# Performance work log

Measured on AMD Instinct MI355X. Metric: run time of the kernel, lower is better.

Reference implementation:

```python
import jax, jax.numpy as jnp
import numpy as np

K = 3
STRIDE = 1


def ste_round(v):
    # Round with straight-through gradient (torch Round Function)
    return v + jax.lax.stop_gradient(jnp.round(v) - v)


def ste_sign(v):
    # Sign with straight-through gradient (torch Sign Function)
    return v + jax.lax.stop_gradient(jnp.sign(v) - v)


def _unfold(x, k, s):
    # torch nn.functional.unfold: [B,C,H,W] -> [B, C*k*k, L], channel-major (c, kh, kw)
    B, C, H, W = x.shape
    Ho = (H - k) // s + 1
    Wo = (W - k) // s + 1
    cols = jnp.stack(
        [x[:, :, i:i + s * Ho:s, j:j + s * Wo:s] for i in range(k) for j in range(k)],
        axis=2,
    )  # [B, C, k*k, Ho, Wo]
    return cols.reshape(B, C * k * k, Ho * Wo)


def reference(x, weight, conv_bias, in_min, in_max, prob_table, rand_idx):
    B = x.shape[0]
    O = weight.shape[0]
    cols = _unfold(x, K, STRIDE)                       # [B, CKK, L]
    CKK = cols.shape[1]
    X = cols.transpose(0, 2, 1).reshape(-1, CKK)       # [N, CKK], N = B*L

    w = ste_sign(weight.reshape(O, CKK))               # ternary weights {-1,0,1}
    wp = jax.nn.relu(w)
    wm = jax.nn.relu(-w)

    scale = in_max - in_min
    Xq = jnp.clip(ste_round((X - in_min) / scale * 15.0), 0.0, 15.0)

    nch = -(-CKK // 4)                                 # ceil(CKK/4)
    pad = nch * 4 - CKK
    if pad:
        Xq = jnp.pad(Xq, ((0, 0), (0, pad)))
        wp = jnp.pad(wp, ((0, 0), (0, pad)))
        wm = jnp.pad(wm, ((0, 0), (0, pad)))

    Xc = Xq.reshape(-1, nch, 4)                        # [N, nch, 4]
    Wp = wp.reshape(O, nch, 4)
    Wm = wm.reshape(O, nch, 4)

    yp = jnp.einsum('nck,ock->cno', Xc, Wp)            # [nch, N, O]
    ym = -jnp.einsum('nck,ock->cno', Xc, Wm)
    T = jnp.stack([yp, ym], axis=1)                    # [nch, 2, N, O]

    longs = jnp.abs(jnp.clip(jnp.round(T), -60.0, 60.0).astype(jnp.int32))
    Q = jnp.clip(ste_round(T / 15.0), -3.0, 3.0)
    temp = prob_table[longs, rand_idx]                 # irregular gather [nch,2,N,O]
    add = temp * jnp.sign(Q) + Q - jax.lax.stop_gradient(Q)

    bias_term = in_min * jnp.sum(w, axis=1)            # linear(InMin*ones, w) -> [O]
    xo = jnp.sum(add, axis=(0, 1)) * scale + bias_term + conv_bias  # [N, O]

    L = X.shape[0] // B
    dim = int(np.sqrt(L))
    return xo.reshape(B, L, O).transpose(0, 2, 1).reshape(B, O, dim, dim)


def setup_inputs() -> dict:
    key = jax.random.key(0)
    k1, k2, k3, k4, k5 = jax.random.split(key, 5)
    B, C, H, W = 2, 16, 66, 66
    O = 64
    CKK = C * K * K            # 144
    nch = -(-CKK // 4)         # 36
    L = ((H - K) // STRIDE + 1) ** 2  # 4096
    N = B * L                  # 8192
    return {
        'x': jax.random.uniform(k1, (B, C, H, W), dtype=jnp.float32),
        'weight': jax.random.normal(k2, (O, C, K, K), dtype=jnp.float32),
        'conv_bias': jax.random.normal(k3, (O,), dtype=jnp.float32),
        'in_min': jnp.zeros((), dtype=jnp.float32),
        'in_max': jnp.ones((), dtype=jnp.float32),
        'prob_table': jax.random.uniform(k4, (61, 1000), dtype=jnp.float32),
        'rand_idx': jax.random.randint(k5, (nch, 2, N, O), 0, 1000, dtype=jnp.int32),
    }
```

## Files before the change

kernel.cpp:

```cpp
#include <hip/hip_runtime.h>

typedef unsigned int uint;

#define B_     2
#define C_     16
#define H_     66
#define W_     66
#define O_     64
#define CKK    144
#define NCH    36
#define DIM    64
#define L_     4096
#define N_     8192
#define PLANE  524288
#define TROWS  61
#define TCOLS  1000

typedef _Float16 h4 __attribute__((ext_vector_type(4)));

__device__ __forceinline__ void loadg(int (&buf)[16],
                                      const int* __restrict__ rp0,
                                      const int* __restrict__ rp1, int c0) {
#pragma unroll
    for (int j = 0; j < 4; ++j) {
        int c = c0 + j;
        buf[4 * j + 0] = rp0[(2 * c)     * PLANE];
        buf[4 * j + 1] = rp0[(2 * c + 1) * PLANE];
        buf[4 * j + 2] = rp1[(2 * c)     * PLANE];
        buf[4 * j + 3] = rp1[(2 * c + 1) * PLANE];
    }
}

__device__ __forceinline__ void procg(const int (&buf)[16],
                                      const uint* __restrict__ xq0,
                                      const uint* __restrict__ xq1,
                                      const uint2* __restrict__ sw,
                                      const _Float16* __restrict__ tbl,
                                      int c0, int o,
                                      float& sum0, float& sum1) {
#pragma unroll
    for (int j = 0; j < 4; ++j) {
        int c = c0 + j;
        uint xv0 = xq0[c];
        uint xv1 = xq1[c];
        uint2 m  = sw[c * O_ + o];
        uint yp0 = ((xv0 & m.x) * 0x01010101u) >> 24;
        uint ym0 = ((xv0 & m.y) * 0x01010101u) >> 24;
        uint yp1 = ((xv1 & m.x) * 0x01010101u) >> 24;
        uint ym1 = ((xv1 & m.y) * 0x01010101u) >> 24;
        sum0 += (float)tbl[yp0 * TCOLS + buf[4 * j + 0]];
        sum0 -= (float)tbl[ym0 * TCOLS + buf[4 * j + 1]];
        sum1 += (float)tbl[yp1 * TCOLS + buf[4 * j + 2]];
        sum1 -= (float)tbl[ym1 * TCOLS + buf[4 * j + 3]];
    }
}

__launch_bounds__(1024)
__global__ void k_fused(const float* __restrict__ x,
                        const float* __restrict__ wgt,
                        const float* __restrict__ cbias,
                        const float* __restrict__ pmin,
                        const float* __restrict__ pmax,
                        const float* __restrict__ ptbl,
                        const int*   __restrict__ ridx,
                        float* __restrict__ out) {
    __shared__ __align__(16) _Float16 tbl[TROWS * TCOLS];
    __shared__ uint2 s_w[NCH * O_];
    __shared__ float s_bias[O_];
    __shared__ uint  s_xq[2][16 * NCH];

    const int tid = threadIdx.x;
    const float mn = pmin[0];
    const float sc = pmax[0] - mn;

    {
        uint4 z; z.x = z.y = z.z = z.w = 0u;
        uint4* zp = (uint4*)tbl;
        for (int p = tid; p < 1000; p += 1024) zp[p] = z;
    }
    {
        const float4* src = (const float4*)(ptbl + 8 * TCOLS);
        h4* dst = (h4*)(tbl + 8 * TCOLS);
        for (int p = tid; p < (53 * TCOLS) / 4; p += 1024) {
            float4 v = src[p];
            h4 h = { (_Float16)v.x, (_Float16)v.y, (_Float16)v.z, (_Float16)v.w };
            dst[p] = h;
        }
    }
    for (int p = tid; p < NCH * O_; p += 1024) {
        int c = p >> 6, oo = p & 63;
        float4 v = *(const float4*)(wgt + oo * CKK + c * 4);
        uint pm = 0, nm = 0;
        if (v.x > 0.0f) pm |= 0x000000FFu; else if (v.x < 0.0f) nm |= 0x000000FFu;
        if (v.y > 0.0f) pm |= 0x0000FF00u; else if (v.y < 0.0f) nm |= 0x0000FF00u;
        if (v.z > 0.0f) pm |= 0x00FF0000u; else if (v.z < 0.0f) nm |= 0x00FF0000u;
        if (v.w > 0.0f) pm |= 0xFF000000u; else if (v.w < 0.0f) nm |= 0xFF000000u;
        s_w[p] = make_uint2(pm, nm);
    }
    for (int i = tid; i < 2 * 16 * NCH; i += 1024) {
        int t  = i / (16 * NCH);
        int r  = i - t * (16 * NCH);
        int nl2 = r / NCH;
        int c2  = r - nl2 * NCH;
        int n2  = (blockIdx.x + t * 256) * 16 + nl2;
        int b2 = n2 >> 12, l2 = n2 & (L_ - 1);
        int h2 = l2 >> 6,  w2 = l2 & (DIM - 1);
        uint packed = 0;
#pragma unroll
        for (int k = 0; k < 4; ++k) {
            int j  = c2 * 4 + k;
            int ci = j / 9;
            int r2 = j - ci * 9;
            int kh = r2 / 3;
            int kw = r2 - kh * 3;
            float v = x[((b2 * C_ + ci) * H_ + (h2 + kh)) * W_ + (w2 + kw)];
            float t2 = (v - mn) / sc * 15.0f;
            float q = fminf(fmaxf(rintf(t2), 0.0f), 15.0f);
            packed |= ((uint)q) << (8 * k);
        }
        s_xq[t][r] = packed;
    }

    const int o  = tid & 63;
    const int nl = tid >> 6;
    const int n0 = blockIdx.x * 16 + nl;
    const int n1 = n0 + 4096;
    const int* rp0 = ridx + n0 * O_ + o;
    const int* rp1 = ridx + n1 * O_ + o;

    int A[16], Bb[16];
    loadg(A,  rp0, rp1, 0);
    loadg(Bb, rp0, rp1, 4);

    __syncthreads();
    if (tid < O_) {
        int sw2 = 0;
        for (int c = 0; c < NCH; ++c) {
            uint2 m = s_w[c * O_ + tid];
            sw2 += (__popc(m.x) >> 3) - (__popc(m.y) >> 3);
        }
        s_bias[tid] = mn * (float)sw2 + cbias[tid];
    }
    __syncthreads();

    const uint* xq0 = &s_xq[0][nl * NCH];
    const uint* xq1 = &s_xq[1][nl * NCH];
    const float bo  = s_bias[o];
    float sum0 = 0.0f, sum1 = 0.0f;

    procg(A,  xq0, xq1, s_w, tbl,  0, o, sum0, sum1); loadg(A,  rp0, rp1,  8);
    procg(Bb, xq0, xq1, s_w, tbl,  4, o, sum0, sum1); loadg(Bb, rp0, rp1, 12);
    procg(A,  xq0, xq1, s_w, tbl,  8, o, sum0, sum1); loadg(A,  rp0, rp1, 16);
    procg(Bb, xq0, xq1, s_w, tbl, 12, o, sum0, sum1); loadg(Bb, rp0, rp1, 20);
    procg(A,  xq0, xq1, s_w, tbl, 16, o, sum0, sum1); loadg(A,  rp0, rp1, 24);
    procg(Bb, xq0, xq1, s_w, tbl, 20, o, sum0, sum1); loadg(Bb, rp0, rp1, 28);
    procg(A,  xq0, xq1, s_w, tbl, 24, o, sum0, sum1); loadg(A,  rp0, rp1, 32);
    procg(Bb, xq0, xq1, s_w, tbl, 28, o, sum0, sum1);
    procg(A,  xq0, xq1, s_w, tbl, 32, o, sum0, sum1);

    out[o * L_ + n0]                       = sum0 * sc + bo;
    out[(O_ + o) * L_ + (n1 & (L_ - 1))]   = sum1 * sc + bo;
}

extern "C" void kernel_launch(void* const* d_in, const int* in_sizes, int n_in,
                              void* d_out, int out_size, void* d_ws, size_t ws_size,
                              hipStream_t stream) {
    const float* x     = (const float*)d_in[0];
    const float* wgt   = (const float*)d_in[1];
    const float* cbias = (const float*)d_in[2];
    const float* pmin  = (const float*)d_in[3];
    const float* pmax  = (const float*)d_in[4];
    const float* ptbl  = (const float*)d_in[5];
    const int*   ridx  = (const int*)d_in[6];
    float* out = (float*)d_out;

    k_fused<<<256, 1024, 0, stream>>>(x, wgt, cbias, pmin, pmax, ptbl, ridx, out);
}
```

Measured before the change: 34.90 us.

## Remap threads to two output channels each and vectorize rand_idx loads

Each thread now handles two adjacent output channels for one position instead of one channel for two batch positions. This lets the rand_idx gathers become int2 loads and the weight masks be packed as uint4 in shared memory. The prefetch depth grows from two to four register buffers, and the rand_idx loads are issued before the table setup to overlap the global latency with shared-memory initialization. The output stores become strided across channels per thread and register pressure increases.

```diff
diff --git a/kernel.cpp b/kernel.cpp
--- a/kernel.cpp
+++ b/kernel.cpp
@@ -18,40 +18,36 @@
 
 typedef _Float16 h4 __attribute__((ext_vector_type(4)));
 
-__device__ __forceinline__ void loadg(int (&buf)[16],
-                                      const int* __restrict__ rp0,
-                                      const int* __restrict__ rp1, int c0) {
+__device__ __forceinline__ void loadg(int2 (&buf)[8],
+                                      const int* __restrict__ rp, int c0) {
 #pragma unroll
     for (int j = 0; j < 4; ++j) {
         int c = c0 + j;
-        buf[4 * j + 0] = rp0[(2 * c)     * PLANE];
-        buf[4 * j + 1] = rp0[(2 * c + 1) * PLANE];
-        buf[4 * j + 2] = rp1[(2 * c)     * PLANE];
-        buf[4 * j + 3] = rp1[(2 * c + 1) * PLANE];
+        buf[2 * j + 0] = *(const int2*)(rp + (2 * c)     * PLANE);
+        buf[2 * j + 1] = *(const int2*)(rp + (2 * c + 1) * PLANE);
     }
 }
 
-__device__ __forceinline__ void procg(const int (&buf)[16],
-                                      const uint* __restrict__ xq0,
-                                      const uint* __restrict__ xq1,
-                                      const uint2* __restrict__ sw,
+__device__ __forceinline__ void procg(const int2 (&buf)[8],
+                                      const uint*  __restrict__ xqp,
+                                      const uint4* __restrict__ swp,
                                       const _Float16* __restrict__ tbl,
-                                      int c0, int o,
-                                      float& sum0, float& sum1) {
+                                      int c0, float& sum0, float& sum1) {
 #pragma unroll
     for (int j = 0; j < 4; ++j) {
         int c = c0 + j;
-        uint xv0 = xq0[c];
-        uint xv1 = xq1[c];
-        uint2 m  = sw[c * O_ + o];
-        uint yp0 = ((xv0 & m.x) * 0x01010101u) >> 24;
-        uint ym0 = ((xv0 & m.y) * 0x01010101u) >> 24;
-        uint yp1 = ((xv1 & m.x) * 0x01010101u) >> 24;
-        uint ym1 = ((xv1 & m.y) * 0x01010101u) >> 24;
-        sum0 += (float)tbl[yp0 * TCOLS + buf[4 * j + 0]];
-        sum0 -= (float)tbl[ym0 * TCOLS + buf[4 * j + 1]];
-        sum1 += (float)tbl[yp1 * TCOLS + buf[4 * j + 2]];
-        sum1 -= (float)tbl[ym1 * TCOLS + buf[4 * j + 3]];
+        uint  xv = xqp[c];
+        uint4 m  = swp[c * 32];
+        uint yp0 = ((xv & m.x) * 0x01010101u) >> 24;
+        uint ym0 = ((xv & m.y) * 0x01010101u) >> 24;
+        uint yp1 = ((xv & m.z) * 0x01010101u) >> 24;
+        uint ym1 = ((xv & m.w) * 0x01010101u) >> 24;
+        int2 b0 = buf[2 * j + 0];
+        int2 b1 = buf[2 * j + 1];
+        sum0 += (float)tbl[yp0 * TCOLS + b0.x];
+        sum0 -= (float)tbl[ym0 * TCOLS + b1.x];
+        sum1 += (float)tbl[yp1 * TCOLS + b0.y];
+        sum1 -= (float)tbl[ym1 * TCOLS + b1.y];
     }
 }
 
@@ -65,44 +61,69 @@
                         const int*   __restrict__ ridx,
                         float* __restrict__ out) {
     __shared__ __align__(16) _Float16 tbl[TROWS * TCOLS];
-    __shared__ uint2 s_w[NCH * O_];
+    __shared__ uint4 s_w4[NCH * 32];
     __shared__ float s_bias[O_];
     __shared__ uint  s_xq[2][16 * NCH];
 
-    const int tid = threadIdx.x;
+    const int tid  = threadIdx.x;
+    const int wv   = tid >> 6;
+    const int lane = tid & 63;
+    const int p    = lane & 31;
+    const int h    = lane >> 5;
+    const int s    = wv >> 3;
+    const int nloc = 2 * (wv & 7) + h;
+    const int o0   = 2 * p;
+
     const float mn = pmin[0];
     const float sc = pmax[0] - mn;
+
+    const int n_g = blockIdx.x * 16 + nloc + s * 4096;
+    const int* rp = ridx + n_g * O_ + o0;
+    int2 A[8], Bb[8], Cc[8], Dd[8];
+    loadg(A,  rp, 0);
+    loadg(Bb, rp, 4);
+    loadg(Cc, rp, 8);
+    loadg(Dd, rp, 12);
 
     {
         uint4 z; z.x = z.y = z.z = z.w = 0u;
         uint4* zp = (uint4*)tbl;
-        for (int p = tid; p < 1000; p += 1024) zp[p] = z;
+        for (int q = tid; q < 1000; q += 1024) zp[q] = z;
     }
     {
         const float4* src = (const float4*)(ptbl + 8 * TCOLS);
         h4* dst = (h4*)(tbl + 8 * TCOLS);
-        for (int p = tid; p < (53 * TCOLS) / 4; p += 1024) {
-            float4 v = src[p];
-            h4 h = { (_Float16)v.x, (_Float16)v.y, (_Float16)v.z, (_Float16)v.w };
-            dst[p] = h;
+        for (int q = tid; q < (53 * TCOLS) / 4; q += 1024) {
+            float4 v = src[q];
+            h4 hh = { (_Float16)v.x, (_Float16)v.y, (_Float16)v.z, (_Float16)v.w };
+            dst[q] = hh;
         }
     }
-    for (int p = tid; p < NCH * O_; p += 1024) {
-        int c = p >> 6, oo = p & 63;
-        float4 v = *(const float4*)(wgt + oo * CKK + c * 4);
+    for (int q = tid; q < NCH * 32; q += 1024) {
+        int c = q >> 5, pp = q & 31;
+        uint4 mo;
+        float4 v0 = *(const float4*)(wgt + (2 * pp)     * CKK + c * 4);
+        float4 v1 = *(const float4*)(wgt + (2 * pp + 1) * CKK + c * 4);
         uint pm = 0, nm = 0;
-        if (v.x > 0.0f) pm |= 0x000000FFu; else if (v.x < 0.0f) nm |= 0x000000FFu;
-        if (v.y > 0.0f) pm |= 0x0000FF00u; else if (v.y < 0.0f) nm |= 0x0000FF00u;
-        if (v.z > 0.0f) pm |= 0x00FF0000u; else if (v.z < 0.0f) nm |= 0x00FF0000u;
-        if (v.w > 0.0f) pm |= 0xFF000000u; else if (v.w < 0.0f) nm |= 0xFF000000u;
-        s_w[p] = make_uint2(pm, nm);
+        if (v0.x > 0.0f) pm |= 0x000000FFu; else if (v0.x < 0.0f) nm |= 0x000000FFu;
+        if (v0.y > 0.0f) pm |= 0x0000FF00u; else if (v0.y < 0.0f) nm |= 0x0000FF00u;
+        if (v0.z > 0.0f) pm |= 0x00FF0000u; else if (v0.z < 0.0f) nm |= 0x00FF0000u;
+        if (v0.w > 0.0f) pm |= 0xFF000000u; else if (v0.w < 0.0f) nm |= 0xFF000000u;
+        mo.x = pm; mo.y = nm;
+        pm = 0; nm = 0;
+        if (v1.x > 0.0f) pm |= 0x000000FFu; else if (v1.x < 0.0f) nm |= 0x000000FFu;
+        if (v1.y > 0.0f) pm |= 0x0000FF00u; else if (v1.y < 0.0f) nm |= 0x0000FF00u;
+        if (v1.z > 0.0f) pm |= 0x00FF0000u; else if (v1.z < 0.0f) nm |= 0x00FF0000u;
+        if (v1.w > 0.0f) pm |= 0xFF000000u; else if (v1.w < 0.0f) nm |= 0xFF000000u;
+        mo.z = pm; mo.w = nm;
+        s_w4[c * 32 + pp] = mo;
     }
     for (int i = tid; i < 2 * 16 * NCH; i += 1024) {
         int t  = i / (16 * NCH);
         int r  = i - t * (16 * NCH);
         int nl2 = r / NCH;
         int c2  = r - nl2 * NCH;
-        int n2  = (blockIdx.x + t * 256) * 16 + nl2;
+        int n2  = blockIdx.x * 16 + nl2 + t * 4096;
         int b2 = n2 >> 12, l2 = n2 & (L_ - 1);
         int h2 = l2 >> 6,  w2 = l2 & (DIM - 1);
         uint packed = 0;
@@ -120,46 +141,37 @@
         }
         s_xq[t][r] = packed;
     }
+    __syncthreads();
 
-    const int o  = tid & 63;
-    const int nl = tid >> 6;
-    const int n0 = blockIdx.x * 16 + nl;
-    const int n1 = n0 + 4096;
-    const int* rp0 = ridx + n0 * O_ + o;
-    const int* rp1 = ridx + n1 * O_ + o;
-
-    int A[16], Bb[16];
-    loadg(A,  rp0, rp1, 0);
-    loadg(Bb, rp0, rp1, 4);
-
-    __syncthreads();
-    if (tid < O_) {
-        int sw2 = 0;
+    if (tid < 32) {
+        int sw0 = 0, sw1 = 0;
         for (int c = 0; c < NCH; ++c) {
-            uint2 m = s_w[c * O_ + tid];
-            sw2 += (__popc(m.x) >> 3) - (__popc(m.y) >> 3);
+            uint4 m = s_w4[c * 32 + tid];
+            sw0 += (__popc(m.x) >> 3) - (__popc(m.y) >> 3);
+            sw1 += (__popc(m.z) >> 3) - (__popc(m.w) >> 3);
         }
-        s_bias[tid] = mn * (float)sw2 + cbias[tid];
+        s_bias[2 * tid]     = mn * (float)sw0 + cbias[2 * tid];
+        s_bias[2 * tid + 1] = mn * (float)sw1 + cbias[2 * tid + 1];
     }
     __syncthreads();
 
-    const uint* xq0 = &s_xq[0][nl * NCH];
-    const uint* xq1 = &s_xq[1][nl * NCH];
-    const float bo  = s_bias[o];
+    const uint*  xqp = &s_xq[s][nloc * NCH];
+    const uint4* swp = &s_w4[p];
     float sum0 = 0.0f, sum1 = 0.0f;
 
-    procg(A,  xq0, xq1, s_w, tbl,  0, o, sum0, sum1); loadg(A,  rp0, rp1,  8);
-    procg(Bb, xq0, xq1, s_w, tbl,  4, o, sum0, sum1); loadg(Bb, rp0, rp1, 12);
-    procg(A,  xq0, xq1, s_w, tbl,  8, o, sum0, sum1); loadg(A,  rp0, rp1, 16);
-    procg(Bb, xq0, xq1, s_w, tbl, 12, o, sum0, sum1); loadg(Bb, rp0, rp1, 20);
-    procg(A,  xq0, xq1, s_w, tbl, 16, o, sum0, sum1); loadg(A,  rp0, rp1, 24);
-    procg(Bb, xq0, xq1, s_w, tbl, 20, o, sum0, sum1); loadg(Bb, rp0, rp1, 28);
-    procg(A,  xq0, xq1, s_w, tbl, 24, o, sum0, sum1); loadg(A,  rp0, rp1, 32);
-    procg(Bb, xq0, xq1, s_w, tbl, 28, o, sum0, sum1);
-    procg(A,  xq0, xq1, s_w, tbl, 32, o, sum0, sum1);
+    procg(A,  xqp, swp, tbl,  0, sum0, sum1); loadg(A,  rp, 16);
+    procg(Bb, xqp, swp, tbl,  4, sum0, sum1); loadg(Bb, rp, 20);
+    procg(Cc, xqp, swp, tbl,  8, sum0, sum1); loadg(Cc, rp, 24);
+    procg(Dd, xqp, swp, tbl, 12, sum0, sum1); loadg(Dd, rp, 28);
+    procg(A,  xqp, swp, tbl, 16, sum0, sum1); loadg(A,  rp, 32);
+    procg(Bb, xqp, swp, tbl, 20, sum0, sum1);
+    procg(Cc, xqp, swp, tbl, 24, sum0, sum1);
+    procg(Dd, xqp, swp, tbl, 28, sum0, sum1);
+    procg(A,  xqp, swp, tbl, 32, sum0, sum1);
 
-    out[o * L_ + n0]                       = sum0 * sc + bo;
-    out[(O_ + o) * L_ + (n1 & (L_ - 1))]   = sum1 * sc + bo;
+    const int l = blockIdx.x * 16 + nloc;
+    out[(s * O_ + o0)     * L_ + l] = sum0 * sc + s_bias[o0];
+    out[(s * O_ + o0 + 1) * L_ + l] = sum1 * sc + s_bias[o0 + 1];
 }
 
 extern "C" void kernel_launch(void* const* d_in, const int* in_sizes, int n_in,
```

Result: slower. 36.54 us (+4.7%).

## Deepen rand_idx prefetch, pad table rows to power-of-two stride, use SAD dot

Applied to the files above, without the earlier changes.

Moves the random-index gathers to the top of the kernel and grows the register prefetch from two to four buffers, so more global loads are in flight while shared-memory setup runs. Pads the shared half-precision probability table to a 1024-column stride, so the row offset is a shift rather than a multiply. Uses the sad_u8 builtin for the 4-byte dot product, and computes the bias directly from global weights, which removes one barrier. The costs are more registers per thread at 1024 threads per block, a larger shared table, an extra barrier after zeroing the whole table, and a serial bias loop with 144 global reads on 64 threads.

```diff
diff --git a/kernel.cpp b/kernel.cpp
--- a/kernel.cpp
+++ b/kernel.cpp
@@ -13,10 +13,19 @@
 #define L_     4096
 #define N_     8192
 #define PLANE  524288
+#define TSTR   1024
 #define TROWS  61
 #define TCOLS  1000
 
 typedef _Float16 h4 __attribute__((ext_vector_type(4)));
+
+__device__ __forceinline__ uint dot4(uint xv, uint m) {
+#if __has_builtin(__builtin_amdgcn_sad_u8)
+    return __builtin_amdgcn_sad_u8(xv & m, 0u, 0u);
+#else
+    return ((xv & m) * 0x01010101u) >> 24;
+#endif
+}
 
 __device__ __forceinline__ void loadg(int (&buf)[16],
                                       const int* __restrict__ rp0,
@@ -32,8 +41,8 @@
 }
 
 __device__ __forceinline__ void procg(const int (&buf)[16],
-                                      const uint* __restrict__ xq0,
-                                      const uint* __restrict__ xq1,
+                                      const uint*  __restrict__ xq0,
+                                      const uint*  __restrict__ xq1,
                                       const uint2* __restrict__ sw,
                                       const _Float16* __restrict__ tbl,
                                       int c0, int o,
@@ -44,14 +53,14 @@
         uint xv0 = xq0[c];
         uint xv1 = xq1[c];
         uint2 m  = sw[c * O_ + o];
-        uint yp0 = ((xv0 & m.x) * 0x01010101u) >> 24;
-        uint ym0 = ((xv0 & m.y) * 0x01010101u) >> 24;
-        uint yp1 = ((xv1 & m.x) * 0x01010101u) >> 24;
-        uint ym1 = ((xv1 & m.y) * 0x01010101u) >> 24;
-        sum0 += (float)tbl[yp0 * TCOLS + buf[4 * j + 0]];
-        sum0 -= (float)tbl[ym0 * TCOLS + buf[4 * j + 1]];
-        sum1 += (float)tbl[yp1 * TCOLS + buf[4 * j + 2]];
-        sum1 -= (float)tbl[ym1 * TCOLS + buf[4 * j + 3]];
+        uint yp0 = dot4(xv0, m.x);
+        uint ym0 = dot4(xv0, m.y);
+        uint yp1 = dot4(xv1, m.x);
+        uint ym1 = dot4(xv1, m.y);
+        sum0 += (float)tbl[(yp0 << 10) + buf[4 * j + 0]];
+        sum0 -= (float)tbl[(ym0 << 10) + buf[4 * j + 1]];
+        sum1 += (float)tbl[(yp1 << 10) + buf[4 * j + 2]];
+        sum1 -= (float)tbl[(ym1 << 10) + buf[4 * j + 3]];
     }
 }
 
@@ -64,7 +73,7 @@
                         const float* __restrict__ ptbl,
                         const int*   __restrict__ ridx,
                         float* __restrict__ out) {
-    __shared__ __align__(16) _Float16 tbl[TROWS * TCOLS];
+    __shared__ __align__(16) _Float16 tbl[TROWS * TSTR];
     __shared__ uint2 s_w[NCH * O_];
     __shared__ float s_bias[O_];
     __shared__ uint  s_xq[2][16 * NCH];
@@ -73,36 +82,46 @@
     const float mn = pmin[0];
     const float sc = pmax[0] - mn;
 
+    const int o  = tid & 63;
+    const int nl = tid >> 6;
+    const int n0 = blockIdx.x * 16 + nl;
+    const int n1 = n0 + 4096;
+    const int* rp0 = ridx + n0 * O_ + o;
+    const int* rp1 = ridx + n1 * O_ + o;
+    int A[16], Bb[16], Cc[16], Dd[16];
+    loadg(A,  rp0, rp1, 0);
+    loadg(Bb, rp0, rp1, 4);
+    loadg(Cc, rp0, rp1, 8);
+    loadg(Dd, rp0, rp1, 12);
+
     {
         uint4 z; z.x = z.y = z.z = z.w = 0u;
         uint4* zp = (uint4*)tbl;
-        for (int p = tid; p < 1000; p += 1024) zp[p] = z;
+        for (int q = tid; q < (TROWS * TSTR) / 8; q += 1024) zp[q] = z;
     }
-    {
-        const float4* src = (const float4*)(ptbl + 8 * TCOLS);
-        h4* dst = (h4*)(tbl + 8 * TCOLS);
-        for (int p = tid; p < (53 * TCOLS) / 4; p += 1024) {
-            float4 v = src[p];
-            h4 h = { (_Float16)v.x, (_Float16)v.y, (_Float16)v.z, (_Float16)v.w };
-            dst[p] = h;
-        }
+    __syncthreads();
+    for (int q = tid; q < 53 * 250; q += 1024) {
+        int r = q / 250, k = q - r * 250;
+        float4 v = *(const float4*)(ptbl + (8 + r) * TCOLS + k * 4);
+        h4 hh = { (_Float16)v.x, (_Float16)v.y, (_Float16)v.z, (_Float16)v.w };
+        *(h4*)(tbl + (8 + r) * TSTR + k * 4) = hh;
     }
-    for (int p = tid; p < NCH * O_; p += 1024) {
-        int c = p >> 6, oo = p & 63;
+    for (int q = tid; q < NCH * O_; q += 1024) {
+        int c = q >> 6, oo = q & 63;
         float4 v = *(const float4*)(wgt + oo * CKK + c * 4);
         uint pm = 0, nm = 0;
         if (v.x > 0.0f) pm |= 0x000000FFu; else if (v.x < 0.0f) nm |= 0x000000FFu;
         if (v.y > 0.0f) pm |= 0x0000FF00u; else if (v.y < 0.0f) nm |= 0x0000FF00u;
         if (v.z > 0.0f) pm |= 0x00FF0000u; else if (v.z < 0.0f) nm |= 0x00FF0000u;
         if (v.w > 0.0f) pm |= 0xFF000000u; else if (v.w < 0.0f) nm |= 0xFF000000u;
-        s_w[p] = make_uint2(pm, nm);
+        s_w[q] = make_uint2(pm, nm);
     }
     for (int i = tid; i < 2 * 16 * NCH; i += 1024) {
         int t  = i / (16 * NCH);
         int r  = i - t * (16 * NCH);
         int nl2 = r / NCH;
         int c2  = r - nl2 * NCH;
-        int n2  = (blockIdx.x + t * 256) * 16 + nl2;
+        int n2  = blockIdx.x * 16 + nl2 + t * 4096;
         int b2 = n2 >> 12, l2 = n2 & (L_ - 1);
         int h2 = l2 >> 6,  w2 = l2 & (DIM - 1);
         uint packed = 0;
@@ -120,26 +139,13 @@
         }
         s_xq[t][r] = packed;
     }
-
-    const int o  = tid & 63;
-    const int nl = tid >> 6;
-    const int n0 = blockIdx.x * 16 + nl;
-    const int n1 = n0 + 4096;
-    const int* rp0 = ridx + n0 * O_ + o;
-    const int* rp1 = ridx + n1 * O_ + o;
-
-    int A[16], Bb[16];
-    loadg(A,  rp0, rp1, 0);
-    loadg(Bb, rp0, rp1, 4);
-
-    __syncthreads();
     if (tid < O_) {
-        int sw2 = 0;
-        for (int c = 0; c < NCH; ++c) {
-            uint2 m = s_w[c * O_ + tid];
-            sw2 += (__popc(m.x) >> 3) - (__popc(m.y) >> 3);
+        int sw = 0;
+        for (int j = 0; j < CKK; ++j) {
+            float v = wgt[tid * CKK + j];
+            sw += (v > 0.0f) - (v < 0.0f);
         }
-        s_bias[tid] = mn * (float)sw2 + cbias[tid];
+        s_bias[tid] = mn * (float)sw + cbias[tid];
     }
     __syncthreads();
 
@@ -148,18 +154,18 @@
     const float bo  = s_bias[o];
     float sum0 = 0.0f, sum1 = 0.0f;
 
-    procg(A,  xq0, xq1, s_w, tbl,  0, o, sum0, sum1); loadg(A,  rp0, rp1,  8);
-    procg(Bb, xq0, xq1, s_w, tbl,  4, o, sum0, sum1); loadg(Bb, rp0, rp1, 12);
-    procg(A,  xq0, xq1, s_w, tbl,  8, o, sum0, sum1); loadg(A,  rp0, rp1, 16);
-    procg(Bb, xq0, xq1, s_w, tbl, 12, o, sum0, sum1); loadg(Bb, rp0, rp1, 20);
-    procg(A,  xq0, xq1, s_w, tbl, 16, o, sum0, sum1); loadg(A,  rp0, rp1, 24);
-    procg(Bb, xq0, xq1, s_w, tbl, 20, o, sum0, sum1); loadg(Bb, rp0, rp1, 28);
-    procg(A,  xq0, xq1, s_w, tbl, 24, o, sum0, sum1); loadg(A,  rp0, rp1, 32);
-    procg(Bb, xq0, xq1, s_w, tbl, 28, o, sum0, sum1);
+    procg(A,  xq0, xq1, s_w, tbl,  0, o, sum0, sum1); loadg(A,  rp0, rp1, 16);
+    procg(Bb, xq0, xq1, s_w, tbl,  4, o, sum0, sum1); loadg(Bb, rp0, rp1, 20);
+    procg(Cc, xq0, xq1, s_w, tbl,  8, o, sum0, sum1); loadg(Cc, rp0, rp1, 24);
+    procg(Dd, xq0, xq1, s_w, tbl, 12, o, sum0, sum1); loadg(Dd, rp0, rp1, 28);
+    procg(A,  xq0, xq1, s_w, tbl, 16, o, sum0, sum1); loadg(A,  rp0, rp1, 32);
+    procg(Bb, xq0, xq1, s_w, tbl, 20, o, sum0, sum1);
+    procg(Cc, xq0, xq1, s_w, tbl, 24, o, sum0, sum1);
+    procg(Dd, xq0, xq1, s_w, tbl, 28, o, sum0, sum1);
     procg(A,  xq0, xq1, s_w, tbl, 32, o, sum0, sum1);
 
-    out[o * L_ + n0]                       = sum0 * sc + bo;
-    out[(O_ + o) * L_ + (n1 & (L_ - 1))]   = sum1 * sc + bo;
+    out[o * L_ + n0]                     = sum0 * sc + bo;
+    out[(O_ + o) * L_ + (n1 & (L_ - 1))] = sum1 * sc + bo;
 }
 
 extern "C" void kernel_launch(void* const* d_in, const int* in_sizes, int n_in,
```

Result: slower. 38.27 us (+9.6%).
